# Performance work log

Measured on AMD Instinct MI355X. Metric: run time of the kernel, lower is better.

Reference implementation:

```python
import jax, jax.numpy as jnp
import numpy as np

B, S, D, H, E, TOPK = 4, 2048, 1024, 2048, 8, 2


def setup_inputs() -> dict:
    key = jax.random.key(0)
    ks = jax.random.split(key, 5)
    scale_d = 1.0 / np.sqrt(D)
    scale_h = 1.0 / np.sqrt(H)
    return {
        "hidden_states": jax.random.normal(ks[0], (B, S, D), dtype=jnp.float32),
        "router_w": jax.random.normal(ks[1], (E, D), dtype=jnp.float32) * scale_d,  # logits = x @ router_w.T
        "w_gate": jax.random.normal(ks[2], (E, H, D), dtype=jnp.float32) * scale_d,
        "w_up": jax.random.normal(ks[3], (E, H, D), dtype=jnp.float32) * scale_d,
        "w_down": jax.random.normal(ks[4], (E, D, H), dtype=jnp.float32) * scale_h,
    }


def reference(hidden_states, router_w, w_gate, w_up, w_down):
    b, s, d = hidden_states.shape
    x = hidden_states.reshape(-1, d)                      # [T, D]
    T = x.shape[0]

    router_logits = x @ router_w.T                        # [T, E]
    router_probs = jax.nn.softmax(router_logits.astype(jnp.float32), axis=-1)
    topk_w, topk_idx = jax.lax.top_k(router_probs, TOPK)  # [T, K]
    topk_w = topk_w / jnp.sum(topk_w, axis=-1, keepdims=True)

    # combine[t, e] = renormalized routing weight of token t for expert e (0 if not selected)
    combine = jnp.zeros((T, E), dtype=topk_w.dtype)
    combine = combine.at[jnp.arange(T)[:, None], topk_idx].add(topk_w)

    # Dense all-expert SwiGLU (correctness baseline; combine zeros out unselected experts)
    g = jnp.einsum('td,ehd->teh', x, w_gate)              # [T, E, H]
    u = jnp.einsum('td,ehd->teh', x, w_up)                # [T, E, H]
    h = jax.nn.silu(g) * u                                # [T, E, H]
    y = jnp.einsum('teh,edh->ted', h, w_down)             # [T, E, D]
    out = jnp.einsum('te,ted->td', combine.astype(y.dtype), y)
    return out.reshape(b, s, d)
```

## Files before the change

### kernel.cpp

```cpp
#include <hip/hip_runtime.h>
#include <hip/hip_bf16.h>
#include <stdint.h>

#define T_TOK 8192
#define D_DIM 1024
#define H_DIM 2048
#define E_NUM 8
#define KSEL  2
#define NROWS (T_TOK*KSEL)

#define BM 128
#define BN 128
#define BK 64

typedef __bf16 bf16_t;
typedef bf16_t bf16x8 __attribute__((ext_vector_type(8)));
typedef float  f32x4  __attribute__((ext_vector_type(4)));

__device__ __forceinline__ ushort f2bf(float f) {
    uint32_t u = __builtin_bit_cast(uint32_t, f);
    uint32_t r = (u + 0x7FFFu + ((u >> 16) & 1u)) >> 16;
    return (ushort)r;
}

__global__ __launch_bounds__(256) void convert_kernel(const float* __restrict__ src,
                                                      ushort* __restrict__ dst, int n4) {
    int i = blockIdx.x * 256 + threadIdx.x;
    int stride = gridDim.x * 256;
    for (; i < n4; i += stride) {
        float4 v = *(const float4*)(src + (size_t)i * 4);
        ushort4 o;
        o.x = f2bf(v.x); o.y = f2bf(v.y); o.z = f2bf(v.z); o.w = f2bf(v.w);
        *(ushort4*)(dst + (size_t)i * 4) = o;
    }
}

__global__ __launch_bounds__(256) void router_kernel(const float* __restrict__ x,
                                                     const float* __restrict__ rw,
                                                     ushort* __restrict__ x16,
                                                     int* __restrict__ topk_idx,
                                                     float* __restrict__ topk_w,
                                                     int* __restrict__ cnt) {
    const int wid  = threadIdx.x >> 6;
    const int lane = threadIdx.x & 63;
    const int t = blockIdx.x * 4 + wid;
    const float* xr = x + (size_t)t * D_DIM;

    float acc[E_NUM];
#pragma unroll
    for (int e = 0; e < E_NUM; e++) acc[e] = 0.f;

#pragma unroll
    for (int i = 0; i < 4; i++) {
        int d0 = i * 256 + lane * 4;
        float4 xv = *(const float4*)(xr + d0);
        ushort4 o;
        o.x = f2bf(xv.x); o.y = f2bf(xv.y); o.z = f2bf(xv.z); o.w = f2bf(xv.w);
        *(ushort4*)(x16 + (size_t)t * D_DIM + d0) = o;
#pragma unroll
        for (int e = 0; e < E_NUM; e++) {
            float4 wv = *(const float4*)(rw + e * D_DIM + d0);
            acc[e] += xv.x * wv.x + xv.y * wv.y + xv.z * wv.z + xv.w * wv.w;
        }
    }
#pragma unroll
    for (int e = 0; e < E_NUM; e++) {
#pragma unroll
        for (int s = 32; s > 0; s >>= 1) acc[e] += __shfl_xor(acc[e], s);
    }
    int e1 = 0; float m1 = acc[0];
#pragma unroll
    for (int e = 1; e < E_NUM; e++) if (acc[e] > m1) { m1 = acc[e]; e1 = e; }
    int e2 = -1; float m2 = -INFINITY;
#pragma unroll
    for (int e = 0; e < E_NUM; e++) if (e != e1 && acc[e] > m2) { m2 = acc[e]; e2 = e; }
    float w1 = 1.f / (1.f + expf(m2 - m1));
    float w2 = 1.f - w1;
    if (lane == 0) {
        topk_idx[t * 2 + 0] = e1; topk_idx[t * 2 + 1] = e2;
        topk_w  [t * 2 + 0] = w1; topk_w  [t * 2 + 1] = w2;
        atomicAdd(cnt + e1, 1);
        atomicAdd(cnt + e2, 1);
    }
}

__global__ void prefix_kernel(const int* __restrict__ cnt, int* __restrict__ offs,
                              int* __restrict__ fill) {
    if (threadIdx.x == 0) {
        int s = 0;
        for (int e = 0; e < E_NUM; e++) { offs[e] = s; fill[e] = s; s += cnt[e]; }
        offs[E_NUM] = s;
    }
}

__global__ __launch_bounds__(256) void scatter_kernel(const int* __restrict__ topk_idx,
                                                      const float* __restrict__ topk_w,
                                                      int* __restrict__ fill,
                                                      int* __restrict__ row_token,
                                                      float* __restrict__ row_weight) {
    int t = blockIdx.x * 256 + threadIdx.x;
#pragma unroll
    for (int k = 0; k < KSEL; k++) {
        int e = topk_idx[t * 2 + k];
        float w = topk_w[t * 2 + k];
        int pos = atomicAdd(fill + e, 1);
        row_token[pos] = t;
        row_weight[pos] = w;
    }
}

__global__ __launch_bounds__(512) void gateup_kernel(const ushort* __restrict__ x16,
                                                     const ushort* __restrict__ wg16,
                                                     const ushort* __restrict__ wu16,
                                                     const int* __restrict__ offs,
                                                     const int* __restrict__ row_token,
                                                     ushort* __restrict__ h16) {
    const int e = blockIdx.z;
    const int off_e = offs[e];
    const int n_e = offs[e + 1] - off_e;
    const int m0 = blockIdx.y * BM;
    if (m0 >= n_e) return;
    const int n0 = blockIdx.x * BN;

    __shared__ __align__(16) ushort sA[BM * BK];
    __shared__ __align__(16) ushort sBg[BN * BK];
    __shared__ __align__(16) ushort sBu[BN * BK];
    __shared__ int sTok[BM];

    const int tid = threadIdx.x;
    if (tid < BM) {
        int r = m0 + tid;
        sTok[tid] = row_token[off_e + (r < n_e ? r : n_e - 1)];
    }
    __syncthreads();

    const int srow = tid >> 2;
    const int sq   = tid & 3;
    const int swz  = srow & 7;
    const int c0 = ((2 * sq)     ^ swz) * 8;
    const int c1 = ((2 * sq + 1) ^ swz) * 8;
    ushort* sAw  = &sA [srow * BK];
    ushort* sBgw = &sBg[srow * BK];
    ushort* sBuw = &sBu[srow * BK];

    const ushort* aRow = x16 + (size_t)sTok[srow] * D_DIM + sq * 16;
    const ushort* gRow = wg16 + ((size_t)e * H_DIM + (n0 + srow)) * D_DIM + sq * 16;
    const ushort* uRow = wu16 + ((size_t)e * H_DIM + (n0 + srow)) * D_DIM + sq * 16;

    const int wid = tid >> 6, lane = tid & 63;
    const int wr = wid >> 2, wc = wid & 3;
    const int fr = lane & 15, fq = lane >> 4;

    f32x4 accg[4][2], accu[4][2];
    f32x4 z4 = {0.f, 0.f, 0.f, 0.f};
#pragma unroll
    for (int m = 0; m < 4; m++)
#pragma unroll
        for (int n = 0; n < 2; n++) { accg[m][n] = z4; accu[m][n] = z4; }

    uint4 ra0 = *(const uint4*)(aRow);
    uint4 ra1 = *(const uint4*)(aRow + 8);
    uint4 rg0 = *(const uint4*)(gRow);
    uint4 rg1 = *(const uint4*)(gRow + 8);
    uint4 ru0 = *(const uint4*)(uRow);
    uint4 ru1 = *(const uint4*)(uRow + 8);

    const int NKT = D_DIM / BK;
    for (int kt = 0; kt < NKT; ++kt) {
        *(uint4*)&sAw [c0] = ra0; *(uint4*)&sAw [c1] = ra1;
        *(uint4*)&sBgw[c0] = rg0; *(uint4*)&sBgw[c1] = rg1;
        *(uint4*)&sBuw[c0] = ru0; *(uint4*)&sBuw[c1] = ru1;
        if (kt + 1 < NKT) {
            const ushort* a = aRow + (kt + 1) * BK;
            const ushort* g = gRow + (kt + 1) * BK;
            const ushort* u = uRow + (kt + 1) * BK;
            ra0 = *(const uint4*)(a); ra1 = *(const uint4*)(a + 8);
            rg0 = *(const uint4*)(g); rg1 = *(const uint4*)(g + 8);
            ru0 = *(const uint4*)(u); ru1 = *(const uint4*)(u + 8);
        }
        __syncthreads();
#pragma unroll
        for (int ks = 0; ks < 2; ++ks) {
            bf16x8 af[4], bg[2], bu[2];
#pragma unroll
            for (int m = 0; m < 4; m++) {
                int r = wr * 64 + m * 16 + fr;
                af[m] = *(const bf16x8*)&sA[r * BK + (((ks * 4 + fq) ^ (r & 7)) * 8)];
            }
#pragma unroll
            for (int n = 0; n < 2; n++) {
                int c = wc * 32 + n * 16 + fr;
                int sl = ((ks * 4 + fq) ^ (c & 7)) * 8;
                bg[n] = *(const bf16x8*)&sBg[c * BK + sl];
                bu[n] = *(const bf16x8*)&sBu[c * BK + sl];
            }
#pragma unroll
            for (int m = 0; m < 4; m++)
#pragma unroll
                for (int n = 0; n < 2; n++) {
                    accg[m][n] = __builtin_amdgcn_mfma_f32_16x16x32_bf16(af[m], bg[n], accg[m][n], 0, 0, 0);
                    accu[m][n] = __builtin_amdgcn_mfma_f32_16x16x32_bf16(af[m], bu[n], accu[m][n], 0, 0, 0);
                }
        }
        __syncthreads();
    }

#pragma unroll
    for (int m = 0; m < 4; m++)
#pragma unroll
        for (int n = 0; n < 2; n++) {
            int col = n0 + wc * 32 + n * 16 + fr;
#pragma unroll
            for (int v = 0; v < 4; v++) {
                int grow = m0 + wr * 64 + m * 16 + fq * 4 + v;
                if (grow < n_e) {
                    float g = accg[m][n][v], u = accu[m][n][v];
                    float h = g / (1.f + expf(-g)) * u;
                    h16[(size_t)(off_e + grow) * H_DIM + col] = f2bf(h);
                }
            }
        }
}

__global__ __launch_bounds__(512) void down_kernel(const ushort* __restrict__ h16,
                                                   const ushort* __restrict__ wd16,
                                                   const int* __restrict__ offs,
                                                   const int* __restrict__ row_token,
                                                   const float* __restrict__ row_weight,
                                                   float* __restrict__ out) {
    const int e = blockIdx.z;
    const int off_e = offs[e];
    const int n_e = offs[e + 1] - off_e;
    const int m0 = blockIdx.y * BM;
    if (m0 >= n_e) return;
    const int n0 = blockIdx.x * BN;

    __shared__ __align__(16) ushort sA[BM * BK];
    __shared__ __align__(16) ushort sB[BN * BK];

    const int tid = threadIdx.x;
    const int srow = tid >> 2;
    const int sq   = tid & 3;
    const int swz  = srow & 7;
    const int c0 = ((2 * sq)     ^ swz) * 8;
    const int c1 = ((2 * sq + 1) ^ swz) * 8;
    ushort* sAw = &sA[srow * BK];
    ushort* sBw = &sB[srow * BK];

    int arow = m0 + srow; if (arow >= n_e) arow = n_e - 1;
    const ushort* aRow = h16 + (size_t)(off_e + arow) * H_DIM + sq * 16;
    const ushort* bRow = wd16 + ((size_t)e * D_DIM + (n0 + srow)) * H_DIM + sq * 16;

    const int wid = tid >> 6, lane = tid & 63;
    const int wr = wid >> 2, wc = wid & 3;
    const int fr = lane & 15, fq = lane >> 4;

    f32x4 acc[4][2];
    f32x4 z4 = {0.f, 0.f, 0.f, 0.f};
#pragma unroll
    for (int m = 0; m < 4; m++)
#pragma unroll
        for (int n = 0; n < 2; n++) acc[m][n] = z4;

    uint4 ra0 = *(const uint4*)(aRow);
    uint4 ra1 = *(const uint4*)(aRow + 8);
    uint4 rb0 = *(const uint4*)(bRow);
    uint4 rb1 = *(const uint4*)(bRow + 8);

    const int NKT = H_DIM / BK;
    for (int kt = 0; kt < NKT; ++kt) {
        *(uint4*)&sAw[c0] = ra0; *(uint4*)&sAw[c1] = ra1;
        *(uint4*)&sBw[c0] = rb0; *(uint4*)&sBw[c1] = rb1;
        if (kt + 1 < NKT) {
            const ushort* a = aRow + (kt + 1) * BK;
            const ushort* b = bRow + (kt + 1) * BK;
            ra0 = *(const uint4*)(a); ra1 = *(const uint4*)(a + 8);
            rb0 = *(const uint4*)(b); rb1 = *(const uint4*)(b + 8);
        }
        __syncthreads();
#pragma unroll
        for (int ks = 0; ks < 2; ++ks) {
            bf16x8 af[4], bf[2];
#pragma unroll
            for (int m = 0; m < 4; m++) {
                int r = wr * 64 + m * 16 + fr;
                af[m] = *(const bf16x8*)&sA[r * BK + (((ks * 4 + fq) ^ (r & 7)) * 8)];
            }
#pragma unroll
            for (int n = 0; n < 2; n++) {
                int c = wc * 32 + n * 16 + fr;
                bf[n] = *(const bf16x8*)&sB[c * BK + (((ks * 4 + fq) ^ (c & 7)) * 8)];
            }
#pragma unroll
            for (int m = 0; m < 4; m++)
#pragma unroll
                for (int n = 0; n < 2; n++)
                    acc[m][n] = __builtin_amdgcn_mfma_f32_16x16x32_bf16(af[m], bf[n], acc[m][n], 0, 0, 0);
        }
        __syncthreads();
    }

#pragma unroll
    for (int m = 0; m < 4; m++)
#pragma unroll
        for (int n = 0; n < 2; n++) {
            int col = n0 + wc * 32 + n * 16 + fr;
#pragma unroll
            for (int v = 0; v < 4; v++) {
                int grow = m0 + wr * 64 + m * 16 + fq * 4 + v;
                if (grow < n_e) {
                    int r = off_e + grow;
                    float w = row_weight[r];
                    int tok = row_token[r];
                    atomicAdd(out + (size_t)tok * D_DIM + col, w * acc[m][n][v]);
                }
            }
        }
}

extern "C" void kernel_launch(void* const* d_in, const int* in_sizes, int n_in,
                              void* d_out, int out_size, void* d_ws, size_t ws_size,
                              hipStream_t stream) {
    const float* x  = (const float*)d_in[0];
    const float* rw = (const float*)d_in[1];
    const float* wg = (const float*)d_in[2];
    const float* wu = (const float*)d_in[3];
    const float* wd = (const float*)d_in[4];
    float* out = (float*)d_out;

    char* p = (char*)d_ws;
    size_t off = 0;
    auto alloc = [&](size_t b) { size_t c = off; off = (off + b + 255) & ~(size_t)255; return c; };
    size_t ctrl_o = alloc(256);
    size_t tki_o  = alloc((size_t)T_TOK * KSEL * 4);
    size_t tkw_o  = alloc((size_t)T_TOK * KSEL * 4);
    size_t rtok_o = alloc((size_t)NROWS * 4);
    size_t rwgt_o = alloc((size_t)NROWS * 4);
    size_t x16_o  = alloc((size_t)T_TOK * D_DIM * 2);
    size_t wg16_o = alloc((size_t)E_NUM * H_DIM * D_DIM * 2);
    size_t wu16_o = alloc((size_t)E_NUM * H_DIM * D_DIM * 2);
    size_t wd16_o = alloc((size_t)E_NUM * D_DIM * H_DIM * 2);
    size_t h16_o  = alloc((size_t)NROWS * H_DIM * 2);
    if (off > ws_size) return;

    int*    cnt        = (int*)(p + ctrl_o);
    int*    offs       = (int*)(p + ctrl_o + 64);
    int*    fill       = (int*)(p + ctrl_o + 128);
    int*    topk_idx   = (int*)(p + tki_o);
    float*  topk_w     = (float*)(p + tkw_o);
    int*    row_token  = (int*)(p + rtok_o);
    float*  row_weight = (float*)(p + rwgt_o);
    ushort* x16  = (ushort*)(p + x16_o);
    ushort* wg16 = (ushort*)(p + wg16_o);
    ushort* wu16 = (ushort*)(p + wu16_o);
    ushort* wd16 = (ushort*)(p + wd16_o);
    ushort* h16  = (ushort*)(p + h16_o);

    hipMemsetAsync(p + ctrl_o, 0, 256, stream);
    hipMemsetAsync(d_out, 0, (size_t)out_size * 4, stream);

    const int n4w = (E_NUM * H_DIM * D_DIM) / 4;
    convert_kernel<<<1024, 256, 0, stream>>>(wg, wg16, n4w);
    convert_kernel<<<1024, 256, 0, stream>>>(wu, wu16, n4w);
    convert_kernel<<<1024, 256, 0, stream>>>(wd, wd16, n4w);

    router_kernel<<<T_TOK / 4, 256, 0, stream>>>(x, rw, x16, topk_idx, topk_w, cnt);
    prefix_kernel<<<1, 64, 0, stream>>>(cnt, offs, fill);
    scatter_kernel<<<T_TOK / 256, 256, 0, stream>>>(topk_idx, topk_w, fill, row_token, row_weight);

    gateup_kernel<<<dim3(H_DIM / BN, T_TOK / BM, E_NUM), 512, 0, stream>>>(
        x16, wg16, wu16, offs, row_token, h16);
    down_kernel<<<dim3(D_DIM / BN, T_TOK / BM, E_NUM), 512, 0, stream>>>(
        h16, wd16, offs, row_token, row_weight, out);
}
```

Measured before the change: 808.7 us.

## Use direct global-to-LDS loads and replace atomic scatter with a combine pass

Both GEMM kernels now stage tiles straight from global memory into LDS with global_load_lds, dropping the register round-trip and the software prefetch. The down projection writes per-row fp32 results into a scratch buffer that reuses the gate-weight workspace. A new combine kernel then gathers each token's two expert rows and applies the routing weights, which removes the float atomics and the output memset. The cost is that loads are no longer overlapped with compute across k-steps (single buffer, one sync per step), plus an extra pass over the intermediate output.

```diff
diff --git a/kernel.cpp b/kernel.cpp
--- a/kernel.cpp
+++ b/kernel.cpp
@@ -21,6 +21,12 @@
     uint32_t u = __builtin_bit_cast(uint32_t, f);
     uint32_t r = (u + 0x7FFFu + ((u >> 16) & 1u)) >> 16;
     return (ushort)r;
+}
+
+__device__ __forceinline__ void gload16(const ushort* g, ushort* l) {
+    __builtin_amdgcn_global_load_lds(
+        (const __attribute__((address_space(1))) void*)g,
+        (__attribute__((address_space(3))) void*)l, 16, 0, 0);
 }
 
 __global__ __launch_bounds__(256) void convert_kernel(const float* __restrict__ src,
@@ -94,18 +100,16 @@
 }
 
 __global__ __launch_bounds__(256) void scatter_kernel(const int* __restrict__ topk_idx,
-                                                      const float* __restrict__ topk_w,
                                                       int* __restrict__ fill,
                                                       int* __restrict__ row_token,
-                                                      float* __restrict__ row_weight) {
+                                                      int* __restrict__ rowmap) {
     int t = blockIdx.x * 256 + threadIdx.x;
 #pragma unroll
     for (int k = 0; k < KSEL; k++) {
         int e = topk_idx[t * 2 + k];
-        float w = topk_w[t * 2 + k];
         int pos = atomicAdd(fill + e, 1);
         row_token[pos] = t;
-        row_weight[pos] = w;
+        rowmap[t * 2 + k] = pos;
     }
 }
 
@@ -134,20 +138,23 @@
     }
     __syncthreads();
 
-    const int srow = tid >> 2;
-    const int sq   = tid & 3;
-    const int swz  = srow & 7;
-    const int c0 = ((2 * sq)     ^ swz) * 8;
-    const int c1 = ((2 * sq + 1) ^ swz) * 8;
-    ushort* sAw  = &sA [srow * BK];
-    ushort* sBgw = &sBg[srow * BK];
-    ushort* sBuw = &sBu[srow * BK];
-
-    const ushort* aRow = x16 + (size_t)sTok[srow] * D_DIM + sq * 16;
-    const ushort* gRow = wg16 + ((size_t)e * H_DIM + (n0 + srow)) * D_DIM + sq * 16;
-    const ushort* uRow = wu16 + ((size_t)e * H_DIM + (n0 + srow)) * D_DIM + sq * 16;
-
     const int wid = tid >> 6, lane = tid & 63;
+    const int s0 = wid * 2, s1 = s0 + 1;
+    const int lrow = lane >> 3;
+    const int lcol = lane & 7;
+    const int xc = ((lcol ^ lrow) * 8);
+    const int rA0 = s0 * 8 + lrow, rA1 = s1 * 8 + lrow;
+
+    const ushort* gA0 = x16 + (size_t)sTok[rA0] * D_DIM + xc;
+    const ushort* gA1 = x16 + (size_t)sTok[rA1] * D_DIM + xc;
+    const ushort* gG0 = wg16 + ((size_t)e * H_DIM + n0 + rA0) * D_DIM + xc;
+    const ushort* gG1 = wg16 + ((size_t)e * H_DIM + n0 + rA1) * D_DIM + xc;
+    const ushort* gU0 = wu16 + ((size_t)e * H_DIM + n0 + rA0) * D_DIM + xc;
+    const ushort* gU1 = wu16 + ((size_t)e * H_DIM + n0 + rA1) * D_DIM + xc;
+    ushort* lA0 = sA  + s0 * 512; ushort* lA1 = sA  + s1 * 512;
+    ushort* lG0 = sBg + s0 * 512; ushort* lG1 = sBg + s1 * 512;
+    ushort* lU0 = sBu + s0 * 512; ushort* lU1 = sBu + s1 * 512;
+
     const int wr = wid >> 2, wc = wid & 3;
     const int fr = lane & 15, fq = lane >> 4;
 
@@ -158,26 +165,12 @@
 #pragma unroll
         for (int n = 0; n < 2; n++) { accg[m][n] = z4; accu[m][n] = z4; }
 
-    uint4 ra0 = *(const uint4*)(aRow);
-    uint4 ra1 = *(const uint4*)(aRow + 8);
-    uint4 rg0 = *(const uint4*)(gRow);
-    uint4 rg1 = *(const uint4*)(gRow + 8);
-    uint4 ru0 = *(const uint4*)(uRow);
-    uint4 ru1 = *(const uint4*)(uRow + 8);
-
     const int NKT = D_DIM / BK;
     for (int kt = 0; kt < NKT; ++kt) {
-        *(uint4*)&sAw [c0] = ra0; *(uint4*)&sAw [c1] = ra1;
-        *(uint4*)&sBgw[c0] = rg0; *(uint4*)&sBgw[c1] = rg1;
-        *(uint4*)&sBuw[c0] = ru0; *(uint4*)&sBuw[c1] = ru1;
-        if (kt + 1 < NKT) {
-            const ushort* a = aRow + (kt + 1) * BK;
-            const ushort* g = gRow + (kt + 1) * BK;
-            const ushort* u = uRow + (kt + 1) * BK;
-            ra0 = *(const uint4*)(a); ra1 = *(const uint4*)(a + 8);
-            rg0 = *(const uint4*)(g); rg1 = *(const uint4*)(g + 8);
-            ru0 = *(const uint4*)(u); ru1 = *(const uint4*)(u + 8);
-        }
+        gload16(gA0, lA0); gload16(gA1, lA1);
+        gload16(gG0, lG0); gload16(gG1, lG1);
+        gload16(gU0, lU0); gload16(gU1, lU1);
+        gA0 += BK; gA1 += BK; gG0 += BK; gG1 += BK; gU0 += BK; gU1 += BK;
         __syncthreads();
 #pragma unroll
         for (int ks = 0; ks < 2; ++ks) {
@@ -225,9 +218,7 @@
 __global__ __launch_bounds__(512) void down_kernel(const ushort* __restrict__ h16,
                                                    const ushort* __restrict__ wd16,
                                                    const int* __restrict__ offs,
-                                                   const int* __restrict__ row_token,
-                                                   const float* __restrict__ row_weight,
-                                                   float* __restrict__ out) {
+                                                   float* __restrict__ y) {
     const int e = blockIdx.z;
     const int off_e = offs[e];
     const int n_e = offs[e + 1] - off_e;
@@ -239,19 +230,21 @@
     __shared__ __align__(16) ushort sB[BN * BK];
 
     const int tid = threadIdx.x;
-    const int srow = tid >> 2;
-    const int sq   = tid & 3;
-    const int swz  = srow & 7;
-    const int c0 = ((2 * sq)     ^ swz) * 8;
-    const int c1 = ((2 * sq + 1) ^ swz) * 8;
-    ushort* sAw = &sA[srow * BK];
-    ushort* sBw = &sB[srow * BK];
-
-    int arow = m0 + srow; if (arow >= n_e) arow = n_e - 1;
-    const ushort* aRow = h16 + (size_t)(off_e + arow) * H_DIM + sq * 16;
-    const ushort* bRow = wd16 + ((size_t)e * D_DIM + (n0 + srow)) * H_DIM + sq * 16;
-
     const int wid = tid >> 6, lane = tid & 63;
+    const int s0 = wid * 2, s1 = s0 + 1;
+    const int lrow = lane >> 3;
+    const int lcol = lane & 7;
+    const int xc = ((lcol ^ lrow) * 8);
+    int ar0 = m0 + s0 * 8 + lrow; if (ar0 >= n_e) ar0 = n_e - 1;
+    int ar1 = m0 + s1 * 8 + lrow; if (ar1 >= n_e) ar1 = n_e - 1;
+
+    const ushort* gA0 = h16 + (size_t)(off_e + ar0) * H_DIM + xc;
+    const ushort* gA1 = h16 + (size_t)(off_e + ar1) * H_DIM + xc;
+    const ushort* gB0 = wd16 + ((size_t)e * D_DIM + n0 + s0 * 8 + lrow) * H_DIM + xc;
+    const ushort* gB1 = wd16 + ((size_t)e * D_DIM + n0 + s1 * 8 + lrow) * H_DIM + xc;
+    ushort* lA0 = sA + s0 * 512; ushort* lA1 = sA + s1 * 512;
+    ushort* lB0 = sB + s0 * 512; ushort* lB1 = sB + s1 * 512;
+
     const int wr = wid >> 2, wc = wid & 3;
     const int fr = lane & 15, fq = lane >> 4;
 
@@ -262,21 +255,11 @@
 #pragma unroll
         for (int n = 0; n < 2; n++) acc[m][n] = z4;
 
-    uint4 ra0 = *(const uint4*)(aRow);
-    uint4 ra1 = *(const uint4*)(aRow + 8);
-    uint4 rb0 = *(const uint4*)(bRow);
-    uint4 rb1 = *(const uint4*)(bRow + 8);
-
     const int NKT = H_DIM / BK;
     for (int kt = 0; kt < NKT; ++kt) {
-        *(uint4*)&sAw[c0] = ra0; *(uint4*)&sAw[c1] = ra1;
-        *(uint4*)&sBw[c0] = rb0; *(uint4*)&sBw[c1] = rb1;
-        if (kt + 1 < NKT) {
-            const ushort* a = aRow + (kt + 1) * BK;
-            const ushort* b = bRow + (kt + 1) * BK;
-            ra0 = *(const uint4*)(a); ra1 = *(const uint4*)(a + 8);
-            rb0 = *(const uint4*)(b); rb1 = *(const uint4*)(b + 8);
-        }
+        gload16(gA0, lA0); gload16(gA1, lA1);
+        gload16(gB0, lB0); gload16(gB1, lB1);
+        gA0 += BK; gA1 += BK; gB0 += BK; gB1 += BK;
         __syncthreads();
 #pragma unroll
         for (int ks = 0; ks < 2; ++ks) {
@@ -308,14 +291,28 @@
 #pragma unroll
             for (int v = 0; v < 4; v++) {
                 int grow = m0 + wr * 64 + m * 16 + fq * 4 + v;
-                if (grow < n_e) {
-                    int r = off_e + grow;
-                    float w = row_weight[r];
-                    int tok = row_token[r];
-                    atomicAdd(out + (size_t)tok * D_DIM + col, w * acc[m][n][v]);
-                }
-            }
-        }
+                if (grow < n_e)
+                    y[(size_t)(off_e + grow) * D_DIM + col] = acc[m][n][v];
+            }
+        }
+}
+
+__global__ __launch_bounds__(256) void combine_kernel(const float* __restrict__ y,
+                                                      const int* __restrict__ rowmap,
+                                                      const float* __restrict__ topk_w,
+                                                      float* __restrict__ out) {
+    const int t = blockIdx.x;
+    const int d = threadIdx.x * 4;
+    const int r0 = rowmap[t * 2], r1 = rowmap[t * 2 + 1];
+    const float w0 = topk_w[t * 2], w1 = topk_w[t * 2 + 1];
+    float4 a = *(const float4*)(y + (size_t)r0 * D_DIM + d);
+    float4 b = *(const float4*)(y + (size_t)r1 * D_DIM + d);
+    float4 o;
+    o.x = w0 * a.x + w1 * b.x;
+    o.y = w0 * a.y + w1 * b.y;
+    o.z = w0 * a.z + w1 * b.z;
+    o.w = w0 * a.w + w1 * b.w;
+    *(float4*)(out + (size_t)t * D_DIM + d) = o;
 }
 
 extern "C" void kernel_launch(void* const* d_in, const int* in_sizes, int n_in,
@@ -335,7 +332,7 @@
     size_t tki_o  = alloc((size_t)T_TOK * KSEL * 4);
     size_t tkw_o  = alloc((size_t)T_TOK * KSEL * 4);
     size_t rtok_o = alloc((size_t)NROWS * 4);
-    size_t rwgt_o = alloc((size_t)NROWS * 4);
+    size_t rmap_o = alloc((size_t)NROWS * 4);
     size_t x16_o  = alloc((size_t)T_TOK * D_DIM * 2);
     size_t wg16_o = alloc((size_t)E_NUM * H_DIM * D_DIM * 2);
     size_t wu16_o = alloc((size_t)E_NUM * H_DIM * D_DIM * 2);
@@ -343,21 +340,21 @@
     size_t h16_o  = alloc((size_t)NROWS * H_DIM * 2);
     if (off > ws_size) return;
 
-    int*    cnt        = (int*)(p + ctrl_o);
-    int*    offs       = (int*)(p + ctrl_o + 64);
-    int*    fill       = (int*)(p + ctrl_o + 128);
-    int*    topk_idx   = (int*)(p + tki_o);
-    float*  topk_w     = (float*)(p + tkw_o);
-    int*    row_token  = (int*)(p + rtok_o);
-    float*  row_weight = (float*)(p + rwgt_o);
+    int*    cnt       = (int*)(p + ctrl_o);
+    int*    offs      = (int*)(p + ctrl_o + 64);
+    int*    fill      = (int*)(p + ctrl_o + 128);
+    int*    topk_idx  = (int*)(p + tki_o);
+    float*  topk_w    = (float*)(p + tkw_o);
+    int*    row_token = (int*)(p + rtok_o);
+    int*    rowmap    = (int*)(p + rmap_o);
     ushort* x16  = (ushort*)(p + x16_o);
     ushort* wg16 = (ushort*)(p + wg16_o);
     ushort* wu16 = (ushort*)(p + wu16_o);
     ushort* wd16 = (ushort*)(p + wd16_o);
     ushort* h16  = (ushort*)(p + h16_o);
+    float*  y    = (float*)(p + wg16_o);
 
     hipMemsetAsync(p + ctrl_o, 0, 256, stream);
-    hipMemsetAsync(d_out, 0, (size_t)out_size * 4, stream);
 
     const int n4w = (E_NUM * H_DIM * D_DIM) / 4;
     convert_kernel<<<1024, 256, 0, stream>>>(wg, wg16, n4w);
@@ -366,10 +363,11 @@
 
     router_kernel<<<T_TOK / 4, 256, 0, stream>>>(x, rw, x16, topk_idx, topk_w, cnt);
     prefix_kernel<<<1, 64, 0, stream>>>(cnt, offs, fill);
-    scatter_kernel<<<T_TOK / 256, 256, 0, stream>>>(topk_idx, topk_w, fill, row_token, row_weight);
+    scatter_kernel<<<T_TOK / 256, 256, 0, stream>>>(topk_idx, fill, row_token, rowmap);
 
     gateup_kernel<<<dim3(H_DIM / BN, T_TOK / BM, E_NUM), 512, 0, stream>>>(
         x16, wg16, wu16, offs, row_token, h16);
     down_kernel<<<dim3(D_DIM / BN, T_TOK / BM, E_NUM), 512, 0, stream>>>(
-        h16, wd16, offs, row_token, row_weight, out);
-}
+        h16, wd16, offs, y);
+    combine_kernel<<<T_TOK, 256, 0, stream>>>(y, rowmap, topk_w, out);
+}
```

Result: slower. 863.0 us (+6.7%).
